# Optimization experiments

Measured on AMD Instinct MI355X. Metric: run time of the kernel, lower is better.

The kernel has to match this reference:

```python
import jax, jax.numpy as jnp
import numpy as np
from jax import lax

INPUT_SIZE = 256
HIDDEN_SIZE = 512
NUM_LAYERS = 2
T = 2048
B = 64


def setup_inputs() -> dict:
    key = jax.random.key(0)
    k1, k2, k3, k4, k5 = jax.random.split(key, 5)
    fan_g = INPUT_SIZE + HIDDEN_SIZE
    inp = {
        "input": jax.random.normal(k1, (T, B, INPUT_SIZE), dtype=jnp.float32),
        "gate_w": jax.random.uniform(k2, (HIDDEN_SIZE, fan_g), dtype=jnp.float32,
                                     minval=-1.0, maxval=1.0) / np.sqrt(fan_g),
        "gate_b": jax.random.uniform(k3, (HIDDEN_SIZE,), dtype=jnp.float32,
                                     minval=-1.0, maxval=1.0) / np.sqrt(fan_g),
        "out_w": jax.random.uniform(k4, (INPUT_SIZE, HIDDEN_SIZE), dtype=jnp.float32,
                                    minval=-1.0, maxval=1.0) / np.sqrt(HIDDEN_SIZE),
        "out_b": jax.random.uniform(k5, (INPUT_SIZE,), dtype=jnp.float32,
                                    minval=-1.0, maxval=1.0) / np.sqrt(HIDDEN_SIZE),
        "name": 0,  # unused forward arg in the original module
    }
    return inp


def reference(input, gate_w, gate_b, out_w, out_b, name):
    # input: [T, B, input_size]
    batch = input.shape[1]
    h0 = jnp.zeros((batch, HIDDEN_SIZE), dtype=jnp.float32)
    c0 = jnp.zeros((batch, HIDDEN_SIZE), dtype=jnp.float32)

    def step(carry, x_t):
        h, c = carry
        combined = jnp.concatenate([h, x_t], axis=1)          # [B, H+I]
        g = combined @ gate_w.T + gate_b
        s = jax.nn.sigmoid(g)                                 # f = i = o = sigmoid(g)
        ch = jnp.tanh(g)                                      # cell_helper
        c = c * s + ch * s
        h = jnp.tanh(c) * s
        return (h, c), None

    carry = (h0, c0)
    # hidden/cell carry over across layers; every layer re-consumes the same input
    for _ in range(NUM_LAYERS):
        carry, _ = lax.scan(step, carry, input)
    h, _ = carry
    output = h @ out_w.T + out_b                              # [B, input_size]
    return output
```

## Files before the change

### kernel.cpp

```cpp
#include <hip/hip_runtime.h>
#include <stdint.h>

#define T_STEPS 2048
#define BATCH   64
#define IN_SZ   256
#define HID     512
#define FANG    768
#define NLAYER  2
#define TOT_STEPS (T_STEPS*NLAYER)

typedef _Float16 h2 __attribute__((ext_vector_type(2)));
typedef unsigned long long u64;
typedef unsigned int u32;

__device__ __forceinline__ float dot2f(h2 a, h2 b, float c) {
#if __has_builtin(__builtin_amdgcn_fdot2)
    return __builtin_amdgcn_fdot2(a, b, c, false);
#else
    return c + (float)a.x * (float)b.x + (float)a.y * (float)b.y;
#endif
}

__device__ __forceinline__ u32 packh2(float a, float b) {
    h2 t{(_Float16)a, (_Float16)b};
    return __builtin_bit_cast(u32, t);
}
__device__ __forceinline__ h2 bch2(float v) { return __builtin_bit_cast(h2, v); }
__device__ __forceinline__ h2 bch2u(u32 v)  { return __builtin_bit_cast(h2, v); }

__device__ __forceinline__ u64 ld_llc(const u64* p) {
    return __hip_atomic_load(p, __ATOMIC_RELAXED, __HIP_MEMORY_SCOPE_AGENT);
}
__device__ __forceinline__ void st_llc(u64* p, u64 v) {
    __hip_atomic_store(p, v, __ATOMIC_RELAXED, __HIP_MEMORY_SCOPE_AGENT);
}

__device__ __forceinline__ void wg_barrier() {
    asm volatile("s_waitcnt lgkmcnt(0)" ::: "memory");
    __builtin_amdgcn_s_barrier();
    asm volatile("" ::: "memory");
}

template<int CTRL>
__device__ __forceinline__ float dpp_add(float x) {
    int xi = __builtin_bit_cast(int, x);
    int yi = __builtin_amdgcn_update_dpp(0, xi, CTRL, 0xf, 0xf, true);
    return x + __builtin_bit_cast(float, yi);
}
__device__ __forceinline__ float reduce16(float x) {
    x = dpp_add<0xB1>(x);
    x = dpp_add<0x4E>(x);
    x = dpp_add<0x124>(x);
    x = dpp_add<0x128>(x);
    return x;
}

__device__ __forceinline__ float rcpf(float x) { return __builtin_amdgcn_rcpf(x); }
__device__ __forceinline__ float tanh_pos(float ax) {
    float t = __expf(-2.0f * ax);
    return (1.0f - t) * rcpf(1.0f + t);
}

__global__ __launch_bounds__(256) void xproj_kernel(
    const float* __restrict__ input,
    const float* __restrict__ gate_w,
    const float* __restrict__ gate_b,
    u32* __restrict__ xp16)
{
    __shared__ _Float16 Bs[64][264];
    __shared__ _Float16 As[64][264];

    const int jt = blockIdx.x;
    const int mg = blockIdx.y;
    const int tid = threadIdx.x;
    const int tx = tid & 15, ty = tid >> 4;
    const int j0 = jt * 64;

    #pragma unroll
    for (int l = 0; l < 16; ++l) {
        int e = tid + l * 256;
        int i = e >> 6, kq = e & 63;
        float4 v = *(const float4*)&gate_w[(size_t)(j0 + i) * FANG + HID + kq * 4];
        *(h2*)&Bs[i][kq * 4]     = h2{(_Float16)v.x, (_Float16)v.y};
        *(h2*)&Bs[i][kq * 4 + 2] = h2{(_Float16)v.z, (_Float16)v.w};
    }

    const float4 gb = *(const float4*)&gate_b[j0 + tx * 4];

    for (int mt = 0; mt < 32; ++mt) {
        const int m0 = (mg * 32 + mt) * 64;
        __syncthreads();
        #pragma unroll
        for (int l = 0; l < 16; ++l) {
            int e = tid + l * 256;
            int i = e >> 6, kq = e & 63;
            float4 v = *(const float4*)&input[(size_t)(m0 + i) * IN_SZ + kq * 4];
            *(h2*)&As[i][kq * 4]     = h2{(_Float16)v.x, (_Float16)v.y};
            *(h2*)&As[i][kq * 4 + 2] = h2{(_Float16)v.z, (_Float16)v.w};
        }
        __syncthreads();

        float acc[4][4] = {};
        #pragma unroll
        for (int q = 0; q < 32; ++q) {
            const int k = ((q + tx) & 31) * 8;
            float4 av[4], bv[4];
            #pragma unroll
            for (int i = 0; i < 4; ++i)  av[i] = *(const float4*)&As[ty * 4 + i][k];
            #pragma unroll
            for (int jj = 0; jj < 4; ++jj) bv[jj] = *(const float4*)&Bs[tx * 4 + jj][k];
            #pragma unroll
            for (int i = 0; i < 4; ++i) {
                h2 a0 = bch2(av[i].x), a1 = bch2(av[i].y);
                h2 a2 = bch2(av[i].z), a3 = bch2(av[i].w);
                #pragma unroll
                for (int jj = 0; jj < 4; ++jj) {
                    acc[i][jj] = dot2f(a0, bch2(bv[jj].x), acc[i][jj]);
                    acc[i][jj] = dot2f(a1, bch2(bv[jj].y), acc[i][jj]);
                    acc[i][jj] = dot2f(a2, bch2(bv[jj].z), acc[i][jj]);
                    acc[i][jj] = dot2f(a3, bch2(bv[jj].w), acc[i][jj]);
                }
            }
        }

        #pragma unroll
        for (int i = 0; i < 4; ++i) {
            uint2 ww = { packh2(acc[i][0] + gb.x, acc[i][1] + gb.y),
                         packh2(acc[i][2] + gb.z, acc[i][3] + gb.w) };
            *(uint2*)&xp16[(size_t)(m0 + ty * 4 + i) * 256 + ((j0 + tx * 4) >> 1)] = ww;
        }
    }
}

__global__ __launch_bounds__(512, 2) void lstm_kernel(
    const float* __restrict__ gate_w,
    const u32* __restrict__ xp16,
    u64* __restrict__ hx)
{
    const int blk  = blockIdx.x;
    const int s    = blk >> 6;
    const int b    = blk & 63;
    const int tid  = threadIdx.x;
    const int g    = tid >> 4;
    const int c    = tid & 15;
    const int wv   = tid >> 6;
    const int lane = tid & 63;
    const int j0   = s * 128 + g * 4;

    __shared__ u32 hl[2][256];

    h2 w2[64];
    #pragma unroll
    for (int u = 0; u < 4; ++u) {
        const int kb = (((s + u) & 3) * 64 + c * 4) * 2;
        #pragma unroll
        for (int rr = 0; rr < 4; ++rr) {
            const float* wr = gate_w + (size_t)(j0 + rr) * FANG + kb;
            float4 v0 = *(const float4*)(wr);
            float4 v1 = *(const float4*)(wr + 4);
            w2[rr * 16 + u * 4 + 0] = h2{(_Float16)v0.x, (_Float16)v0.y};
            w2[rr * 16 + u * 4 + 1] = h2{(_Float16)v0.z, (_Float16)v0.w};
            w2[rr * 16 + u * 4 + 2] = h2{(_Float16)v1.x, (_Float16)v1.y};
            w2[rr * 16 + u * 4 + 3] = h2{(_Float16)v1.z, (_Float16)v1.w};
        }
    }

    const bool poller = (lane < 24);
    const int  pi  = wv * 24 + lane;
    const int  si  = pi >> 6;
    const int  qs  = si + (si >= s);
    const int  prw = qs * 64 + (pi & 63);

    if (tid < 256) hl[0][tid] = 0;

    float cval = 0.0f;

    for (int st = 0; st < TOT_STEPS; ++st) {
        const int t   = st & (T_STEPS - 1);
        const int buf = st & 1;

        u32 xw = 0;
        if (c < 4) xw = xp16[((size_t)t * BATCH + b) * 256 + s * 64 + g * 2 + (c >> 1)];

        const u64* pp = hx + ((size_t)buf * BATCH + b) * 256 + prw;
        u64 pv = 0;
        if (poller) pv = ld_llc(pp);

        wg_barrier();

        float a0 = 0.f, a1 = 0.f, a2 = 0.f, a3 = 0.f;
        {
            float4 rv = *(const float4*)&hl[buf][s * 64 + c * 4];
            h2 x0 = bch2(rv.x), x1 = bch2(rv.y), x2 = bch2(rv.z), x3 = bch2(rv.w);
            a0 = dot2f(w2[ 0], x0, a0); a0 = dot2f(w2[ 1], x1, a0);
            a0 = dot2f(w2[ 2], x2, a0); a0 = dot2f(w2[ 3], x3, a0);
            a1 = dot2f(w2[16], x0, a1); a1 = dot2f(w2[17], x1, a1);
            a1 = dot2f(w2[18], x2, a1); a1 = dot2f(w2[19], x3, a1);
            a2 = dot2f(w2[32], x0, a2); a2 = dot2f(w2[33], x1, a2);
            a2 = dot2f(w2[34], x2, a2); a2 = dot2f(w2[35], x3, a2);
            a3 = dot2f(w2[48], x0, a3); a3 = dot2f(w2[49], x1, a3);
            a3 = dot2f(w2[50], x2, a3); a3 = dot2f(w2[51], x3, a3);
        }

        if (poller) {
            u64 v = pv;
            int spin = 0;
            while ((u32)(v >> 32) != (u32)st) {
                v = ld_llc(pp);
                if (++spin > (1 << 16)) break;
                if (spin > 64) __builtin_amdgcn_s_sleep(1);
            }
            hl[buf][prw] = (u32)v;
        }
        wg_barrier();

        #pragma unroll
        for (int u = 1; u < 4; ++u) {
            float4 rv = *(const float4*)&hl[buf][((s + u) & 3) * 64 + c * 4];
            h2 x0 = bch2(rv.x), x1 = bch2(rv.y), x2 = bch2(rv.z), x3 = bch2(rv.w);
            a0 = dot2f(w2[     u*4+0], x0, a0); a0 = dot2f(w2[     u*4+1], x1, a0);
            a0 = dot2f(w2[     u*4+2], x2, a0); a0 = dot2f(w2[     u*4+3], x3, a0);
            a1 = dot2f(w2[16 + u*4+0], x0, a1); a1 = dot2f(w2[16 + u*4+1], x1, a1);
            a1 = dot2f(w2[16 + u*4+2], x2, a1); a1 = dot2f(w2[16 + u*4+3], x3, a1);
            a2 = dot2f(w2[32 + u*4+0], x0, a2); a2 = dot2f(w2[32 + u*4+1], x1, a2);
            a2 = dot2f(w2[32 + u*4+2], x2, a2); a2 = dot2f(w2[32 + u*4+3], x3, a2);
            a3 = dot2f(w2[48 + u*4+0], x0, a3); a3 = dot2f(w2[48 + u*4+1], x1, a3);
            a3 = dot2f(w2[48 + u*4+2], x2, a3); a3 = dot2f(w2[48 + u*4+3], x3, a3);
        }

        a0 = reduce16(a0);
        a1 = reduce16(a1);
        a2 = reduce16(a2);
        a3 = reduce16(a3);

        float hf = 0.0f;
        if (c < 4) {
            float p = (c == 0) ? a0 : (c == 1) ? a1 : (c == 2) ? a2 : a3;
            h2 xp = bch2u(xw);
            float gg = p + (float)((c & 1) ? xp.y : xp.x);
            float et = __expf(-gg);
            float sg = rcpf(1.0f + et);
            float ch = copysignf(tanh_pos(fabsf(gg)), gg);
            cval = (cval + ch) * sg;
            float th = copysignf(tanh_pos(fabsf(cval)), cval);
            hf = th * sg;
        }
        float hfo = __shfl_down(hf, 1);
        if (c == 0 || c == 2) {
            const int w = s * 64 + g * 2 + (c >> 1);
            u32 pk = packh2(hf, hfo);
            st_llc(hx + ((size_t)((st + 1) & 1) * BATCH + b) * 256 + w,
                   (u64)pk | ((u64)(u32)(st + 1) << 32));
            hl[buf ^ 1][w] = pk;
        }
    }
}

__global__ __launch_bounds__(256) void out_kernel(
    const u64* __restrict__ hx,
    const float* __restrict__ out_w,
    const float* __restrict__ out_b,
    float* __restrict__ out)
{
    const int b  = blockIdx.x;
    const int jt = threadIdx.x;
    __shared__ float hrow[512];

    {
        u64 v = hx[(size_t)b * 256 + jt];
        h2 pr = bch2u((u32)v);
        hrow[2 * jt]     = (float)pr.x;
        hrow[2 * jt + 1] = (float)pr.y;
    }
    __syncthreads();

    float acc = out_b[jt];
    const float* wr = out_w + (size_t)jt * HID;
    #pragma unroll 8
    for (int k = 0; k < HID; ++k)
        acc += hrow[k] * wr[k];
    out[(size_t)b * IN_SZ + jt] = acc;
}

extern "C" void kernel_launch(void* const* d_in, const int* in_sizes, int n_in,
                              void* d_out, int out_size, void* d_ws, size_t ws_size,
                              hipStream_t stream)
{
    const float* input  = (const float*)d_in[0];
    const float* gate_w = (const float*)d_in[1];
    const float* gate_b = (const float*)d_in[2];
    const float* out_w  = (const float*)d_in[3];
    const float* out_b  = (const float*)d_in[4];
    float* out = (float*)d_out;

    u32* xp16 = (u32*)d_ws;
    const size_t xbytes = (size_t)T_STEPS * BATCH * 256 * sizeof(u32);
    u64* hx = (u64*)((char*)d_ws + xbytes);

    (void)hipMemsetAsync(hx, 0, (size_t)2 * BATCH * 256 * sizeof(u64), stream);

    dim3 g1(8, 64);
    xproj_kernel<<<g1, 256, 0, stream>>>(input, gate_w, gate_b, xp16);
    lstm_kernel<<<256, 512, 0, stream>>>(gate_w, xp16, hx);
    out_kernel<<<64, 256, 0, stream>>>(hx, out_w, out_b, out);
}
```

Measured before the change: 5.064 ms.

## Rewrite input projection GEMM with MFMA f16 instructions

Replaces the LDS-tiled dot2 input-projection kernel with an MFMA 16x16x32 f16 version. Each wave holds two 16-row A fragments in registers and streams gate_w rows straight from global memory, converting them to f16 on the fly. This aims to cut the time of the precompute GEMM by using matrix cores instead of scalar dot2 ALU work. In exchange, B operands are re-read from global/L2 by every block without LDS reuse, and outputs are written as scattered 2-byte stores. The output layout (row-major f16 over 512 columns) matches the previous packed layout.

Result: faster. 4.891 ms, median of 2 (-3.4%).

```diff
diff --git a/kernel.cpp b/kernel.cpp
--- a/kernel.cpp
+++ b/kernel.cpp
@@ -10,6 +10,8 @@
 #define TOT_STEPS (T_STEPS*NLAYER)
 
 typedef _Float16 h2 __attribute__((ext_vector_type(2)));
+typedef _Float16 f16x8 __attribute__((ext_vector_type(8)));
+typedef float    f32x4 __attribute__((ext_vector_type(4)));
 typedef unsigned long long u64;
 typedef unsigned int u32;
 
@@ -61,73 +63,56 @@
     return (1.0f - t) * rcpf(1.0f + t);
 }
 
-__global__ __launch_bounds__(256) void xproj_kernel(
+__global__ __launch_bounds__(256, 4) void xproj_kernel(
     const float* __restrict__ input,
     const float* __restrict__ gate_w,
     const float* __restrict__ gate_b,
-    u32* __restrict__ xp16)
-{
-    __shared__ _Float16 Bs[64][264];
-    __shared__ _Float16 As[64][264];
-
-    const int jt = blockIdx.x;
-    const int mg = blockIdx.y;
-    const int tid = threadIdx.x;
-    const int tx = tid & 15, ty = tid >> 4;
-    const int j0 = jt * 64;
-
-    #pragma unroll
-    for (int l = 0; l < 16; ++l) {
-        int e = tid + l * 256;
-        int i = e >> 6, kq = e & 63;
-        float4 v = *(const float4*)&gate_w[(size_t)(j0 + i) * FANG + HID + kq * 4];
-        *(h2*)&Bs[i][kq * 4]     = h2{(_Float16)v.x, (_Float16)v.y};
-        *(h2*)&Bs[i][kq * 4 + 2] = h2{(_Float16)v.z, (_Float16)v.w};
-    }
-
-    const float4 gb = *(const float4*)&gate_b[j0 + tx * 4];
-
-    for (int mt = 0; mt < 32; ++mt) {
-        const int m0 = (mg * 32 + mt) * 64;
-        __syncthreads();
-        #pragma unroll
-        for (int l = 0; l < 16; ++l) {
-            int e = tid + l * 256;
-            int i = e >> 6, kq = e & 63;
-            float4 v = *(const float4*)&input[(size_t)(m0 + i) * IN_SZ + kq * 4];
-            *(h2*)&As[i][kq * 4]     = h2{(_Float16)v.x, (_Float16)v.y};
-            *(h2*)&As[i][kq * 4 + 2] = h2{(_Float16)v.z, (_Float16)v.w};
-        }
-        __syncthreads();
-
-        float acc[4][4] = {};
-        #pragma unroll
-        for (int q = 0; q < 32; ++q) {
-            const int k = ((q + tx) & 31) * 8;
-            float4 av[4], bv[4];
-            #pragma unroll
-            for (int i = 0; i < 4; ++i)  av[i] = *(const float4*)&As[ty * 4 + i][k];
-            #pragma unroll
-            for (int jj = 0; jj < 4; ++jj) bv[jj] = *(const float4*)&Bs[tx * 4 + jj][k];
-            #pragma unroll
-            for (int i = 0; i < 4; ++i) {
-                h2 a0 = bch2(av[i].x), a1 = bch2(av[i].y);
-                h2 a2 = bch2(av[i].z), a3 = bch2(av[i].w);
-                #pragma unroll
-                for (int jj = 0; jj < 4; ++jj) {
-                    acc[i][jj] = dot2f(a0, bch2(bv[jj].x), acc[i][jj]);
-                    acc[i][jj] = dot2f(a1, bch2(bv[jj].y), acc[i][jj]);
-                    acc[i][jj] = dot2f(a2, bch2(bv[jj].z), acc[i][jj]);
-                    acc[i][jj] = dot2f(a3, bch2(bv[jj].w), acc[i][jj]);
-                }
-            }
-        }
-
+    _Float16* __restrict__ xph)
+{
+    const int w    = threadIdx.x >> 6;
+    const int lane = threadIdx.x & 63;
+    const int lr   = lane & 15;
+    const int lg   = lane >> 4;
+    const int m0a  = blockIdx.x * 128 + w * 32;
+    const int m0b  = m0a + 16;
+
+    f16x8 afa[8], afb[8];
+    {
+        const float* ara = input + (size_t)(m0a + lr) * IN_SZ + lg * 8;
+        const float* arb = input + (size_t)(m0b + lr) * IN_SZ + lg * 8;
+        #pragma unroll
+        for (int t = 0; t < 8; ++t) {
+            float4 v0 = *(const float4*)(ara + t * 32);
+            float4 v1 = *(const float4*)(ara + t * 32 + 4);
+            afa[t] = f16x8{(_Float16)v0.x, (_Float16)v0.y, (_Float16)v0.z, (_Float16)v0.w,
+                           (_Float16)v1.x, (_Float16)v1.y, (_Float16)v1.z, (_Float16)v1.w};
+            float4 u0 = *(const float4*)(arb + t * 32);
+            float4 u1 = *(const float4*)(arb + t * 32 + 4);
+            afb[t] = f16x8{(_Float16)u0.x, (_Float16)u0.y, (_Float16)u0.z, (_Float16)u0.w,
+                           (_Float16)u1.x, (_Float16)u1.y, (_Float16)u1.z, (_Float16)u1.w};
+        }
+    }
+
+    for (int n0 = 0; n0 < HID; n0 += 16) {
+        const float* br = gate_w + (size_t)(n0 + lr) * FANG + HID + lg * 8;
+        f32x4 acc_a = {0.f, 0.f, 0.f, 0.f};
+        f32x4 acc_b = {0.f, 0.f, 0.f, 0.f};
+        #pragma unroll
+        for (int t = 0; t < 8; ++t) {
+            float4 v0 = *(const float4*)(br + t * 32);
+            float4 v1 = *(const float4*)(br + t * 32 + 4);
+            f16x8 bf = f16x8{(_Float16)v0.x, (_Float16)v0.y, (_Float16)v0.z, (_Float16)v0.w,
+                             (_Float16)v1.x, (_Float16)v1.y, (_Float16)v1.z, (_Float16)v1.w};
+            acc_a = __builtin_amdgcn_mfma_f32_16x16x32_f16(afa[t], bf, acc_a, 0, 0, 0);
+            acc_b = __builtin_amdgcn_mfma_f32_16x16x32_f16(afb[t], bf, acc_b, 0, 0, 0);
+        }
+        const float gb = gate_b[n0 + lr];
         #pragma unroll
         for (int i = 0; i < 4; ++i) {
-            uint2 ww = { packh2(acc[i][0] + gb.x, acc[i][1] + gb.y),
-                         packh2(acc[i][2] + gb.z, acc[i][3] + gb.w) };
-            *(uint2*)&xp16[(size_t)(m0 + ty * 4 + i) * 256 + ((j0 + tx * 4) >> 1)] = ww;
+            const int ra = m0a + lg * 4 + i;
+            const int rb = m0b + lg * 4 + i;
+            xph[(size_t)ra * HID + n0 + lr] = (_Float16)(acc_a[i] + gb);
+            xph[(size_t)rb * HID + n0 + lr] = (_Float16)(acc_b[i] + gb);
         }
     }
 }
@@ -293,14 +278,14 @@
     const float* out_b  = (const float*)d_in[4];
     float* out = (float*)d_out;
 
-    u32* xp16 = (u32*)d_ws;
-    const size_t xbytes = (size_t)T_STEPS * BATCH * 256 * sizeof(u32);
+    _Float16* xph = (_Float16*)d_ws;
+    u32*      xp16 = (u32*)d_ws;
+    const size_t xbytes = (size_t)T_STEPS * BATCH * HID * sizeof(_Float16);
     u64* hx = (u64*)((char*)d_ws + xbytes);
 
     (void)hipMemsetAsync(hx, 0, (size_t)2 * BATCH * 256 * sizeof(u64), stream);
 
-    dim3 g1(8, 64);
-    xproj_kernel<<<g1, 256, 0, stream>>>(input, gate_w, gate_b, xp16);
+    xproj_kernel<<<1024, 256, 0, stream>>>(input, gate_w, gate_b, xph);
     lstm_kernel<<<256, 512, 0, stream>>>(gate_w, xp16, hx);
     out_kernel<<<64, 256, 0, stream>>>(hx, out_w, out_b, out);
 }
```
